# Kernel optimization log

Measured on AMD Instinct MI355X. Metric: run time of the kernel, lower is better.

Reference implementation:

```python
import jax, jax.numpy as jnp
import numpy as np

EMBED_DIM = 1024
NUM_HEADS = 16
HEAD_DIM = EMBED_DIM // NUM_HEADS
THETA = 10000.0


def setup_inputs() -> dict:
    key = jax.random.key(0)
    ks = jax.random.split(key, 5)
    B, S, E = 2, 2048, EMBED_DIM
    x = jax.random.normal(ks[0], (B, S, E), dtype=jnp.float32)
    s = 1.0 / np.sqrt(E)
    Wq = jax.random.normal(ks[1], (E, E), dtype=jnp.float32) * s
    Wk = jax.random.normal(ks[2], (E, E), dtype=jnp.float32) * s
    Wv = jax.random.normal(ks[3], (E, E), dtype=jnp.float32) * s
    Wo = jax.random.normal(ks[4], (E, E), dtype=jnp.float32) * s
    bo = jnp.zeros((E,), dtype=jnp.float32)
    return {"x": x, "Wq": Wq, "Wk": Wk, "Wv": Wv, "Wo": Wo, "bo": bo}


def _apply_rope(t, cos, sin):
    # t: (B, H, S, D); cos, sin: (S, D/2)
    t1 = t[..., 0::2]
    t2 = t[..., 1::2]
    r1 = t1 * cos - t2 * sin
    r2 = t1 * sin + t2 * cos
    # interleave back: (..., D/2, 2) -> (..., D)
    return jnp.stack([r1, r2], axis=-1).reshape(t.shape)


def reference(x, Wq, Wk, Wv, Wo, bo):
    B, S, E = x.shape
    H, D = NUM_HEADS, HEAD_DIM
    scale = D ** -0.5

    # projections (torch Linear: y = x @ W.T)
    q = (x @ Wq.T).reshape(B, S, H, D).transpose(0, 2, 1, 3)
    k = (x @ Wk.T).reshape(B, S, H, D).transpose(0, 2, 1, 3)
    v = (x @ Wv.T).reshape(B, S, H, D).transpose(0, 2, 1, 3)

    # fixed RoPE freqs (temporal, non-learned)
    freqs = 1.0 / THETA ** (jnp.arange(0, D, 2, dtype=jnp.float32) / D)  # (D/2,)
    pos = jnp.arange(S, dtype=jnp.float32)
    angles = pos[:, None] * freqs[None, :]  # (S, D/2)
    cos, sin = jnp.cos(angles), jnp.sin(angles)

    q = _apply_rope(q, cos, sin)
    k = _apply_rope(k, cos, sin)

    attn = jnp.einsum('bhqd,bhkd->bhqk', q, k) * scale
    attn = jax.nn.softmax(attn, axis=-1)
    out = jnp.einsum('bhqk,bhkd->bhqd', attn, v)
    out = out.transpose(0, 2, 1, 3).reshape(B, S, E)
    return out @ Wo.T + bo
```

## Files before the change

### kernel.cpp

```cpp
#include <hip/hip_runtime.h>


typedef __attribute__((ext_vector_type(8))) short bf16x8;
typedef __attribute__((ext_vector_type(4))) float f32x4;
typedef unsigned short u16;
typedef unsigned int u32;

#define MFMA(a, b, c) __builtin_amdgcn_mfma_f32_16x16x32_bf16((a), (b), (c), 0, 0, 0)

#define GLOAD16(g, l)                                                        \
  __builtin_amdgcn_global_load_lds((const __attribute__((address_space(1))) void*)(g), \
                                   (__attribute__((address_space(3))) void*)(l), 16, 0, 0)

__device__ __forceinline__ float bf2f(u16 u) {
  union { u32 i; float f; } v; v.i = ((u32)u) << 16; return v.f;
}
__device__ __forceinline__ u16 f2bf(float f) {
  union { float f; u32 i; } v; v.f = f;
  u32 x = v.i;
  return (u16)((x + 0x7fffu + ((x >> 16) & 1u)) >> 16);
}
__device__ __forceinline__ float exp2a(float x) {
  float y;
  asm("v_exp_f32 %0, %1" : "=v"(y) : "v"(x));
  return y;
}
__device__ __forceinline__ u32 cvtpk(float a, float b) {
  u32 w;
  asm("v_cvt_pk_bf16_f32 %0, %1, %2" : "=v"(w) : "v"(a), "v"(b));
  return w;
}

__global__ __launch_bounds__(256) void prep_kernel(
    const float* __restrict__ x, const float* __restrict__ Wq, const float* __restrict__ Wk,
    const float* __restrict__ Wv, const float* __restrict__ Wo, u16* __restrict__ xb,
    u16* __restrict__ Wqb, u16* __restrict__ Wkb, u16* __restrict__ Wvb, u16* __restrict__ Wob,
    float* __restrict__ cosT, float* __restrict__ sinT) {
  int bid = blockIdx.x;
  if (bid < 4096) {
    int i = bid * 256 + threadIdx.x;
    const float* src;
    u16* dst;
    int r, sel;
    if (i < 524288) {
      src = x; dst = xb; r = i; sel = -1;
    } else {
      int k = i - 524288;
      sel = k >> 17;
      r = k & 131071;
      src = sel == 0 ? Wq : sel == 1 ? Wk : sel == 2 ? Wv : Wo;
      dst = sel == 0 ? Wqb : sel == 1 ? Wkb : sel == 2 ? Wvb : Wob;
    }
    const float4* p = (const float4*)src + 2 * (size_t)r;
    float4 a = p[0], b = p[1];
    bf16x8 o;
    o[0] = (short)f2bf(a.x); o[1] = (short)f2bf(a.y);
    o[2] = (short)f2bf(a.z); o[3] = (short)f2bf(a.w);
    o[4] = (short)f2bf(b.x); o[5] = (short)f2bf(b.y);
    o[6] = (short)f2bf(b.z); o[7] = (short)f2bf(b.w);
    int outr = r;
    if (sel == 0 || sel == 1) {
      int row = r >> 7, kc = r & 127;
      int h = row >> 6, dd = row & 63;
      int u = dd & 1, pp = dd >> 1, half = pp >> 4, c = pp & 15;
      int g = 16 * (2 * half + u) + c;
      outr = (h * 64 + g) * 128 + kc;
    }
    *(bf16x8*)(dst + 8 * (size_t)outr) = o;
  } else {
    int i = (bid - 4096) * 256 + threadIdx.x;
    int p = i >> 11, s = i & 2047;
    float freq = powf(10000.0f, -(float)(2 * p) / 64.0f);
    float ang = (float)s * freq;
    cosT[i] = cosf(ang);
    sinT[i] = sinf(ang);
  }
}

template <int MODE>
__global__ __launch_bounds__(256) void gemm_bt_kernel(
    const u16* __restrict__ A, const u16* __restrict__ B0, const u16* __restrict__ B1,
    const u16* __restrict__ B2, u16* __restrict__ Qo, u16* __restrict__ Ko,
    u16* __restrict__ VT, const float* __restrict__ cosT, const float* __restrict__ sinT,
    float* __restrict__ Cf, const float* __restrict__ bias, int Ntot) {
  const int K = 1024;
  const int tid = threadIdx.x, lane = tid & 63, wid = tid >> 6;
  const int wr = wid >> 1, wc = wid & 1;
  const int wg = blockIdx.y * gridDim.x + blockIdx.x;
  const int xcd = wg & 7, loc = wg >> 3;
  const int mt = xcd * 4 + (loc & 3);
  const int nt = loc >> 2;
  const int m0 = mt * 128;
  const int n0 = nt * 128;
  const u16* Bt;
  int nloc0, sel;
  if (MODE == 0) {
    sel = nt >> 3;
    Bt = sel == 0 ? B0 : (sel == 1 ? B1 : B2);
    nloc0 = n0 & 1023;
  } else {
    sel = 0;
    Bt = B0;
    nloc0 = n0;
  }

  constexpr int NB = (MODE == 1) ? 2 : 1;
  __shared__ u16 As[NB][128 * 64];
  __shared__ u16 Bs[NB][128 * 64];

  f32x4 acc[4][4];
#pragma unroll
  for (int i = 0; i < 4; i++)
#pragma unroll
    for (int j = 0; j < 4; j++) acc[i][j] = f32x4{0.f, 0.f, 0.f, 0.f};

  const int strow = tid >> 3;
  const int sgcol0 = (tid & 7) * 8;

  auto stage = [&](int k0, int bf) {
#pragma unroll
    for (int p = 0; p < 4; ++p) {
      int row = p * 32 + strow;
      int gcol = sgcol0 ^ ((row & 7) << 3);
      const u16* ga = A + (size_t)(m0 + row) * K + k0 + gcol;
      const u16* gb = Bt + (size_t)(nloc0 + row) * K + k0 + gcol;
      u16* la = As[bf] + (p * 256 + wid * 64) * 8;
      u16* lb = Bs[bf] + (p * 256 + wid * 64) * 8;
      GLOAD16(ga, la);
      GLOAD16(gb, lb);
    }
  };

  auto compute = [&](int bf) {
#pragma unroll
    for (int kk = 0; kk < 2; ++kk) {
      bf16x8 af[4], bfr[4];
#pragma unroll
      for (int i = 0; i < 4; ++i) {
        int row = wr * 64 + i * 16 + (lane & 15);
        int col = (kk * 32 + (lane >> 4) * 8) ^ ((row & 7) << 3);
        af[i] = *(const bf16x8*)(As[bf] + row * 64 + col);
      }
#pragma unroll
      for (int j = 0; j < 4; ++j) {
        int row = wc * 64 + j * 16 + (lane & 15);
        int col = (kk * 32 + (lane >> 4) * 8) ^ ((row & 7) << 3);
        bfr[j] = *(const bf16x8*)(Bs[bf] + row * 64 + col);
      }
#pragma unroll
      for (int i = 0; i < 4; ++i)
#pragma unroll
        for (int j = 0; j < 4; ++j) acc[i][j] = MFMA(af[i], bfr[j], acc[i][j]);
    }
  };

  if (MODE == 1) {
    stage(0, 0);
    for (int kt = 0; kt < 16; ++kt) {
      __syncthreads();
      if (kt + 1 < 16) stage((kt + 1) * 64, (kt + 1) & 1);
      compute(kt & 1);
    }
  } else {
    for (int k0 = 0; k0 < K; k0 += 64) {
      stage(k0, 0);
      __syncthreads();
      compute(0);
      __syncthreads();
    }
  }

  if (MODE == 1) {
#pragma unroll
    for (int i = 0; i < 4; ++i)
#pragma unroll
      for (int j = 0; j < 4; ++j)
#pragma unroll
        for (int r = 0; r < 4; ++r) {
          int row = m0 + wr * 64 + i * 16 + (lane >> 4) * 4 + r;
          int col = n0 + wc * 64 + j * 16 + (lane & 15);
          Cf[(size_t)row * Ntot + col] = acc[i][j][r] + bias[col];
        }
    return;
  }

  const int c = lane & 15;
  const int hh = (nloc0 + wc * 64) >> 6;
  if (sel < 2) {
    u16* dst = sel == 0 ? Qo : Ko;
    const float mul = sel == 0 ? 0.18033688f : 1.0f;
#pragma unroll
    for (int i = 0; i < 4; ++i) {
      int rowb = m0 + wr * 64 + i * 16 + (lane >> 4) * 4;
      int s = rowb & 2047, b = rowb >> 11;
      size_t obase = ((size_t)(b * 16 + hh) * 2048 + s) * 64;
#pragma unroll
      for (int half = 0; half < 2; ++half) {
        int p = half * 16 + c;
        float4 c4 = *(const float4*)(cosT + p * 2048 + s);
        float4 s4 = *(const float4*)(sinT + p * 2048 + s);
#pragma unroll
        for (int r = 0; r < 4; ++r) {
          float t1 = acc[i][2 * half][r], t2 = acc[i][2 * half + 1][r];
          float cc = (&c4.x)[r], ss = (&s4.x)[r];
          float r0 = (t1 * cc - t2 * ss) * mul;
          float r1 = (t1 * ss + t2 * cc) * mul;
          u32 pk = (u32)f2bf(r0) | ((u32)f2bf(r1) << 16);
          *(u32*)(dst + obase + (size_t)r * 64 + 2 * p) = pk;
        }
      }
    }
  } else {
#pragma unroll
    for (int i = 0; i < 4; ++i) {
      int rowb = m0 + wr * 64 + i * 16 + (lane >> 4) * 4;
      int s = rowb & 2047, b = rowb >> 11;
#pragma unroll
      for (int j = 0; j < 4; ++j) {
        int dd = j * 16 + c;
        ushort4 pk;
        pk.x = f2bf(acc[i][j][0]);
        pk.y = f2bf(acc[i][j][1]);
        pk.z = f2bf(acc[i][j][2]);
        pk.w = f2bf(acc[i][j][3]);
        *(ushort4*)(VT + ((size_t)(b * 16 + hh) * 64 + dd) * 2048 + s) = pk;
      }
    }
  }
}

__global__ __launch_bounds__(256) void attn_kernel(
    const u16* __restrict__ Q, const u16* __restrict__ Kk, const u16* __restrict__ VT,
    u16* __restrict__ O) {
  const int wg = blockIdx.y * gridDim.x + blockIdx.x;
  const int xcd = wg & 7, loc = wg >> 3;
  const int qt = loc & 15;
  const int bh = xcd * 4 + (loc >> 4);
  const int tid = threadIdx.x, lane = tid & 63, wid = tid >> 6;
  const int b = bh >> 4, h = bh & 15;
  const int hi = lane >> 4, c = lane & 15;
  const float CEXP = 34.6246810f;

  __shared__ u16 Ks[2][64 * 64];
  __shared__ u16 Vs[2][64 * 64];
  __shared__ char Ps[4][16 * 288];

  const int qrow0 = qt * 128 + wid * 32;
  bf16x8 qf[2][2];
#pragma unroll
  for (int g = 0; g < 2; ++g) {
    const size_t qbase = ((size_t)bh * 2048 + qrow0 + g * 16 + c) * 64;
    qf[g][0] = *(const bf16x8*)(Q + qbase + hi * 8);
    qf[g][1] = *(const bf16x8*)(Q + qbase + 32 + hi * 8);
  }

  f32x4 o[2][4];
#pragma unroll
  for (int g = 0; g < 2; ++g)
#pragma unroll
    for (int j = 0; j < 4; ++j) o[g][j] = f32x4{0.f, 0.f, 0.f, 0.f};
  float lsum[2] = {0.f, 0.f};

  const u16* Kb = Kk + (size_t)bh * 2048 * 64;
  const u16* Vb = VT + (size_t)bh * 64 * 2048;

  const int strow = tid >> 3;
  const int sgc0 = (tid & 7) * 8;
  auto stage = [&](int t, int buf) {
#pragma unroll
    for (int p = 0; p < 2; ++p) {
      int row = p * 32 + strow;
      int gcol = sgc0 ^ ((row & 7) << 3);
      const u16* gk = Kb + (size_t)(t * 64 + row) * 64 + gcol;
      const u16* gv = Vb + (size_t)row * 2048 + t * 64 + gcol;
      u16* lk = Ks[buf] + (p * 256 + wid * 64) * 8;
      u16* lv = Vs[buf] + (p * 256 + wid * 64) * 8;
      GLOAD16(gk, lk);
      GLOAD16(gv, lv);
    }
  };

  stage(0, 0);
  char* Pw = &Ps[wid][0];
  const int pwb = hi * 288 + c * 8;
  const int prb = hi * 576 + c * 8;
  for (int t = 0; t < 32; ++t) {
    const int buf = t & 1;
    __syncthreads();
    if (t + 1 < 32) stage(t + 1, buf ^ 1);

    bf16x8 kf[2][4];
#pragma unroll
    for (int kk = 0; kk < 2; ++kk)
#pragma unroll
      for (int j = 0; j < 4; ++j) {
        int row = j * 16 + c;
        int col = (kk * 32 + hi * 8) ^ ((row & 7) << 3);
        kf[kk][j] = *(const bf16x8*)(Ks[buf] + row * 64 + col);
      }

    f32x4 sc[2][4];
#pragma unroll
    for (int g = 0; g < 2; ++g)
#pragma unroll
      for (int j = 0; j < 4; ++j) sc[g][j] = f32x4{0.f, 0.f, 0.f, 0.f};
    __builtin_amdgcn_s_setprio(1);
#pragma unroll
    for (int kk = 0; kk < 2; ++kk)
#pragma unroll
      for (int g = 0; g < 2; ++g)
#pragma unroll
        for (int j = 0; j < 4; ++j) sc[g][j] = MFMA(kf[kk][j], qf[g][kk], sc[g][j]);
    __builtin_amdgcn_s_setprio(0);

#pragma unroll
    for (int g = 0; g < 2; ++g)
#pragma unroll
      for (int j = 0; j < 4; ++j) {
        float e0 = exp2a(sc[g][j][0] - CEXP);
        float e1 = exp2a(sc[g][j][1] - CEXP);
        float e2 = exp2a(sc[g][j][2] - CEXP);
        float e3 = exp2a(sc[g][j][3] - CEXP);
        lsum[g] += (e0 + e1) + (e2 + e3);
        uint2 w;
        w.x = cvtpk(e0, e1);
        w.y = cvtpk(e2, e3);
        *(uint2*)(Pw + pwb + j * 1152 + g * 128) = w;
      }

    bf16x8 vf[2][4];
#pragma unroll
    for (int kk = 0; kk < 2; ++kk)
#pragma unroll
      for (int j = 0; j < 4; ++j) {
        int vrow = j * 16 + c;
        int vcol = (kk * 32 + hi * 8) ^ ((vrow & 7) << 3);
        vf[kk][j] = *(const bf16x8*)(Vs[buf] + vrow * 64 + vcol);
      }

    __builtin_amdgcn_s_setprio(1);
#pragma unroll
    for (int g = 0; g < 2; ++g)
#pragma unroll
      for (int kk = 0; kk < 2; ++kk) {
        uint2 a = *(const uint2*)(Pw + prb + kk * 2304 + g * 128);
        uint2 bb = *(const uint2*)(Pw + prb + kk * 2304 + g * 128 + 288);
        union { u32 w[4]; bf16x8 v; } pu;
        pu.w[0] = a.x; pu.w[1] = a.y; pu.w[2] = bb.x; pu.w[3] = bb.y;
#pragma unroll
        for (int jd = 0; jd < 4; ++jd) o[g][jd] = MFMA(pu.v, vf[kk][jd], o[g][jd]);
      }
    __builtin_amdgcn_s_setprio(0);
  }

  float linv[2][4];
#pragma unroll
  for (int g = 0; g < 2; ++g) {
    lsum[g] += __shfl_xor(lsum[g], 16, 64);
    lsum[g] += __shfl_xor(lsum[g], 32, 64);
#pragma unroll
    for (int r = 0; r < 4; ++r) {
      float L = __shfl(lsum[g], 4 * hi + r, 64);
      linv[g][r] = __frcp_rn(L);
    }
  }

#pragma unroll
  for (int g = 0; g < 2; ++g)
#pragma unroll
    for (int jd = 0; jd < 4; ++jd)
#pragma unroll
      for (int r = 0; r < 4; ++r) {
        int srow = qrow0 + g * 16 + hi * 4 + r;
        int col = h * 64 + jd * 16 + c;
        float val = o[g][jd][r] * linv[g][r];
        O[(size_t)(b * 2048 + srow) * 1024 + col] = f2bf(val);
      }
}

extern "C" void kernel_launch(void* const* d_in, const int* in_sizes, int n_in,
                              void* d_out, int out_size, void* d_ws, size_t ws_size,
                              hipStream_t stream) {
  const float* x = (const float*)d_in[0];
  const float* Wq = (const float*)d_in[1];
  const float* Wk = (const float*)d_in[2];
  const float* Wv = (const float*)d_in[3];
  const float* Wo = (const float*)d_in[4];
  const float* bo = (const float*)d_in[5];

  char* ws = (char*)d_ws;
  size_t off = 0;
  auto carve = [&](size_t bytes) {
    void* pp = ws + off;
    off += (bytes + 255) & ~(size_t)255;
    return pp;
  };
  u16* xb = (u16*)carve(4194304ull * 2);
  u16* Wqb = (u16*)carve(1048576ull * 2);
  u16* Wkb = (u16*)carve(1048576ull * 2);
  u16* Wvb = (u16*)carve(1048576ull * 2);
  u16* Wob = (u16*)carve(1048576ull * 2);
  float* cosT = (float*)carve(65536ull * 4);
  float* sinT = (float*)carve(65536ull * 4);
  u16* q_r = (u16*)carve(4194304ull * 2);
  u16* k_r = (u16*)carve(4194304ull * 2);
  u16* vT = (u16*)carve(4194304ull * 2);
  u16* attn_out = (u16*)carve(4194304ull * 2);

  prep_kernel<<<4352, 256, 0, stream>>>(x, Wq, Wk, Wv, Wo, xb, Wqb, Wkb, Wvb, Wob, cosT, sinT);
  gemm_bt_kernel<0><<<dim3(24, 32), 256, 0, stream>>>(xb, Wqb, Wkb, Wvb, q_r, k_r, vT, cosT,
                                                      sinT, nullptr, nullptr, 3072);
  attn_kernel<<<dim3(16, 32), 256, 0, stream>>>(q_r, k_r, vT, attn_out);
  gemm_bt_kernel<1><<<dim3(8, 32), 256, 0, stream>>>(attn_out, Wob, nullptr, nullptr, nullptr,
                                                     nullptr, nullptr, nullptr, nullptr,
                                                     (float*)d_out, bo, 1024);
}
```

Baseline: 200.0 us.

## Split out-projection into 64x128-tile kernel and compute softmax row sums via MFMA

Replaces the templated GEMM with a dedicated QKV kernel and a separate output-projection kernel that uses 64x128 tiles and a 512-block grid. The smaller tiles double the workgroup count so more CUs are busy for the 4096x1024 output GEMM. In attention, the exp offset is folded into the accumulator initialisation, and the row sums are computed by an extra MFMA against a ones vector instead of scalar adds plus cross-lane shuffles. This moves VALU and shuffle work onto the matrix unit at the cost of one extra MFMA per P block, and the row sums now come from bf16-rounded probabilities.

```diff
diff --git a/kernel.cpp b/kernel.cpp
--- a/kernel.cpp
+++ b/kernel.cpp
@@ -12,9 +12,6 @@
   __builtin_amdgcn_global_load_lds((const __attribute__((address_space(1))) void*)(g), \
                                    (__attribute__((address_space(3))) void*)(l), 16, 0, 0)
 
-__device__ __forceinline__ float bf2f(u16 u) {
-  union { u32 i; float f; } v; v.i = ((u32)u) << 16; return v.f;
-}
 __device__ __forceinline__ u16 f2bf(float f) {
   union { float f; u32 i; } v; v.f = f;
   u32 x = v.i;
@@ -77,12 +74,10 @@
   }
 }
 
-template <int MODE>
-__global__ __launch_bounds__(256) void gemm_bt_kernel(
+__global__ __launch_bounds__(256) void gemm_qkv_kernel(
     const u16* __restrict__ A, const u16* __restrict__ B0, const u16* __restrict__ B1,
     const u16* __restrict__ B2, u16* __restrict__ Qo, u16* __restrict__ Ko,
-    u16* __restrict__ VT, const float* __restrict__ cosT, const float* __restrict__ sinT,
-    float* __restrict__ Cf, const float* __restrict__ bias, int Ntot) {
+    u16* __restrict__ VT, const float* __restrict__ cosT, const float* __restrict__ sinT) {
   const int K = 1024;
   const int tid = threadIdx.x, lane = tid & 63, wid = tid >> 6;
   const int wr = wid >> 1, wc = wid & 1;
@@ -92,21 +87,12 @@
   const int nt = loc >> 2;
   const int m0 = mt * 128;
   const int n0 = nt * 128;
-  const u16* Bt;
-  int nloc0, sel;
-  if (MODE == 0) {
-    sel = nt >> 3;
-    Bt = sel == 0 ? B0 : (sel == 1 ? B1 : B2);
-    nloc0 = n0 & 1023;
-  } else {
-    sel = 0;
-    Bt = B0;
-    nloc0 = n0;
-  }
-
-  constexpr int NB = (MODE == 1) ? 2 : 1;
-  __shared__ u16 As[NB][128 * 64];
-  __shared__ u16 Bs[NB][128 * 64];
+  const int sel = nt >> 3;
+  const u16* Bt = sel == 0 ? B0 : (sel == 1 ? B1 : B2);
+  const int nloc0 = n0 & 1023;
+
+  __shared__ u16 As[128 * 64];
+  __shared__ u16 Bs[128 * 64];
 
   f32x4 acc[4][4];
 #pragma unroll
@@ -117,21 +103,23 @@
   const int strow = tid >> 3;
   const int sgcol0 = (tid & 7) * 8;
 
-  auto stage = [&](int k0, int bf) {
+  auto stage = [&](int k0) {
 #pragma unroll
     for (int p = 0; p < 4; ++p) {
       int row = p * 32 + strow;
       int gcol = sgcol0 ^ ((row & 7) << 3);
       const u16* ga = A + (size_t)(m0 + row) * K + k0 + gcol;
       const u16* gb = Bt + (size_t)(nloc0 + row) * K + k0 + gcol;
-      u16* la = As[bf] + (p * 256 + wid * 64) * 8;
-      u16* lb = Bs[bf] + (p * 256 + wid * 64) * 8;
+      u16* la = As + (p * 256 + wid * 64) * 8;
+      u16* lb = Bs + (p * 256 + wid * 64) * 8;
       GLOAD16(ga, la);
       GLOAD16(gb, lb);
     }
   };
 
-  auto compute = [&](int bf) {
+  for (int k0 = 0; k0 < K; k0 += 64) {
+    stage(k0);
+    __syncthreads();
 #pragma unroll
     for (int kk = 0; kk < 2; ++kk) {
       bf16x8 af[4], bfr[4];
@@ -139,49 +127,20 @@
       for (int i = 0; i < 4; ++i) {
         int row = wr * 64 + i * 16 + (lane & 15);
         int col = (kk * 32 + (lane >> 4) * 8) ^ ((row & 7) << 3);
-        af[i] = *(const bf16x8*)(As[bf] + row * 64 + col);
+        af[i] = *(const bf16x8*)(As + row * 64 + col);
       }
 #pragma unroll
       for (int j = 0; j < 4; ++j) {
         int row = wc * 64 + j * 16 + (lane & 15);
         int col = (kk * 32 + (lane >> 4) * 8) ^ ((row & 7) << 3);
-        bfr[j] = *(const bf16x8*)(Bs[bf] + row * 64 + col);
+        bfr[j] = *(const bf16x8*)(Bs + row * 64 + col);
       }
 #pragma unroll
       for (int i = 0; i < 4; ++i)
 #pragma unroll
         for (int j = 0; j < 4; ++j) acc[i][j] = MFMA(af[i], bfr[j], acc[i][j]);
     }
-  };
-
-  if (MODE == 1) {
-    stage(0, 0);
-    for (int kt = 0; kt < 16; ++kt) {
-      __syncthreads();
-      if (kt + 1 < 16) stage((kt + 1) * 64, (kt + 1) & 1);
-      compute(kt & 1);
-    }
-  } else {
-    for (int k0 = 0; k0 < K; k0 += 64) {
-      stage(k0, 0);
-      __syncthreads();
-      compute(0);
-      __syncthreads();
-    }
-  }
-
-  if (MODE == 1) {
-#pragma unroll
-    for (int i = 0; i < 4; ++i)
-#pragma unroll
-      for (int j = 0; j < 4; ++j)
-#pragma unroll
-        for (int r = 0; r < 4; ++r) {
-          int row = m0 + wr * 64 + i * 16 + (lane >> 4) * 4 + r;
-          int col = n0 + wc * 64 + j * 16 + (lane & 15);
-          Cf[(size_t)row * Ntot + col] = acc[i][j][r] + bias[col];
-        }
-    return;
+    __syncthreads();
   }
 
   const int c = lane & 15;
@@ -227,6 +186,87 @@
       }
     }
   }
+}
+
+__global__ __launch_bounds__(256) void gemm_out_kernel(
+    const u16* __restrict__ A, const u16* __restrict__ Bw, float* __restrict__ Cf,
+    const float* __restrict__ bias) {
+  const int K = 1024, Ntot = 1024;
+  const int tid = threadIdx.x, lane = tid & 63, wid = tid >> 6;
+  const int wr = wid >> 1, wc = wid & 1;
+  const int wg = blockIdx.x;
+  const int xcd = wg & 7, loc = wg >> 3;
+  const int mt = xcd * 8 + (loc & 7);
+  const int nt = loc >> 3;
+  const int m0 = mt * 64, n0 = nt * 128;
+
+  __shared__ u16 As[2][64 * 64];
+  __shared__ u16 Bs[2][128 * 64];
+
+  f32x4 acc[2][4];
+#pragma unroll
+  for (int i = 0; i < 2; i++)
+#pragma unroll
+    for (int j = 0; j < 4; j++) acc[i][j] = f32x4{0.f, 0.f, 0.f, 0.f};
+
+  const int strow = tid >> 3;
+  const int sgcol0 = (tid & 7) * 8;
+
+  auto stage = [&](int k0, int bf) {
+#pragma unroll
+    for (int p = 0; p < 2; ++p) {
+      int row = p * 32 + strow;
+      int gcol = sgcol0 ^ ((row & 7) << 3);
+      GLOAD16(A + (size_t)(m0 + row) * K + k0 + gcol, As[bf] + (p * 256 + wid * 64) * 8);
+    }
+#pragma unroll
+    for (int p = 0; p < 4; ++p) {
+      int row = p * 32 + strow;
+      int gcol = sgcol0 ^ ((row & 7) << 3);
+      GLOAD16(Bw + (size_t)(n0 + row) * K + k0 + gcol, Bs[bf] + (p * 256 + wid * 64) * 8);
+    }
+  };
+
+  auto compute = [&](int bf) {
+#pragma unroll
+    for (int kk = 0; kk < 2; ++kk) {
+      bf16x8 af[2], bfr[4];
+#pragma unroll
+      for (int i = 0; i < 2; ++i) {
+        int row = wr * 32 + i * 16 + (lane & 15);
+        int col = (kk * 32 + (lane >> 4) * 8) ^ ((row & 7) << 3);
+        af[i] = *(const bf16x8*)(As[bf] + row * 64 + col);
+      }
+#pragma unroll
+      for (int j = 0; j < 4; ++j) {
+        int row = wc * 64 + j * 16 + (lane & 15);
+        int col = (kk * 32 + (lane >> 4) * 8) ^ ((row & 7) << 3);
+        bfr[j] = *(const bf16x8*)(Bs[bf] + row * 64 + col);
+      }
+#pragma unroll
+      for (int i = 0; i < 2; ++i)
+#pragma unroll
+        for (int j = 0; j < 4; ++j) acc[i][j] = MFMA(af[i], bfr[j], acc[i][j]);
+    }
+  };
+
+  stage(0, 0);
+  for (int kt = 0; kt < 16; ++kt) {
+    __syncthreads();
+    if (kt + 1 < 16) stage((kt + 1) * 64, (kt + 1) & 1);
+    compute(kt & 1);
+  }
+
+#pragma unroll
+  for (int i = 0; i < 2; ++i)
+#pragma unroll
+    for (int j = 0; j < 4; ++j)
+#pragma unroll
+      for (int r = 0; r < 4; ++r) {
+        int row = m0 + wr * 32 + i * 16 + (lane >> 4) * 4 + r;
+        int col = n0 + wc * 64 + j * 16 + (lane & 15);
+        Cf[(size_t)row * Ntot + col] = acc[i][j][r] + bias[col];
+      }
 }
 
 __global__ __launch_bounds__(256) void attn_kernel(
@@ -254,12 +294,16 @@
     qf[g][1] = *(const bf16x8*)(Q + qbase + 32 + hi * 8);
   }
 
+  bf16x8 ONES;
+#pragma unroll
+  for (int e = 0; e < 8; ++e) ONES[e] = (short)0x3F80;
+
   f32x4 o[2][4];
 #pragma unroll
   for (int g = 0; g < 2; ++g)
 #pragma unroll
     for (int j = 0; j < 4; ++j) o[g][j] = f32x4{0.f, 0.f, 0.f, 0.f};
-  float lsum[2] = {0.f, 0.f};
+  f32x4 ol[2] = {f32x4{0.f, 0.f, 0.f, 0.f}, f32x4{0.f, 0.f, 0.f, 0.f}};
 
   const u16* Kb = Kk + (size_t)bh * 2048 * 64;
   const u16* Vb = VT + (size_t)bh * 64 * 2048;
@@ -303,7 +347,7 @@
 #pragma unroll
     for (int g = 0; g < 2; ++g)
 #pragma unroll
-      for (int j = 0; j < 4; ++j) sc[g][j] = f32x4{0.f, 0.f, 0.f, 0.f};
+      for (int j = 0; j < 4; ++j) sc[g][j] = f32x4{-CEXP, -CEXP, -CEXP, -CEXP};
     __builtin_amdgcn_s_setprio(1);
 #pragma unroll
     for (int kk = 0; kk < 2; ++kk)
@@ -317,11 +361,10 @@
     for (int g = 0; g < 2; ++g)
 #pragma unroll
       for (int j = 0; j < 4; ++j) {
-        float e0 = exp2a(sc[g][j][0] - CEXP);
-        float e1 = exp2a(sc[g][j][1] - CEXP);
-        float e2 = exp2a(sc[g][j][2] - CEXP);
-        float e3 = exp2a(sc[g][j][3] - CEXP);
-        lsum[g] += (e0 + e1) + (e2 + e3);
+        float e0 = exp2a(sc[g][j][0]);
+        float e1 = exp2a(sc[g][j][1]);
+        float e2 = exp2a(sc[g][j][2]);
+        float e3 = exp2a(sc[g][j][3]);
         uint2 w;
         w.x = cvtpk(e0, e1);
         w.y = cvtpk(e2, e3);
@@ -347,35 +390,28 @@
         uint2 bb = *(const uint2*)(Pw + prb + kk * 2304 + g * 128 + 288);
         union { u32 w[4]; bf16x8 v; } pu;
         pu.w[0] = a.x; pu.w[1] = a.y; pu.w[2] = bb.x; pu.w[3] = bb.y;
+        ol[g] = MFMA(pu.v, ONES, ol[g]);
 #pragma unroll
         for (int jd = 0; jd < 4; ++jd) o[g][jd] = MFMA(pu.v, vf[kk][jd], o[g][jd]);
       }
     __builtin_amdgcn_s_setprio(0);
   }
 
-  float linv[2][4];
 #pragma unroll
   for (int g = 0; g < 2; ++g) {
-    lsum[g] += __shfl_xor(lsum[g], 16, 64);
-    lsum[g] += __shfl_xor(lsum[g], 32, 64);
-#pragma unroll
-    for (int r = 0; r < 4; ++r) {
-      float L = __shfl(lsum[g], 4 * hi + r, 64);
-      linv[g][r] = __frcp_rn(L);
-    }
-  }
-
-#pragma unroll
-  for (int g = 0; g < 2; ++g)
+    float linv[4];
+#pragma unroll
+    for (int r = 0; r < 4; ++r) linv[r] = __frcp_rn(ol[g][r]);
 #pragma unroll
     for (int jd = 0; jd < 4; ++jd)
 #pragma unroll
       for (int r = 0; r < 4; ++r) {
         int srow = qrow0 + g * 16 + hi * 4 + r;
         int col = h * 64 + jd * 16 + c;
-        float val = o[g][jd][r] * linv[g][r];
+        float val = o[g][jd][r] * linv[r];
         O[(size_t)(b * 2048 + srow) * 1024 + col] = f2bf(val);
       }
+  }
 }
 
 extern "C" void kernel_launch(void* const* d_in, const int* in_sizes, int n_in,
@@ -408,10 +444,7 @@
   u16* attn_out = (u16*)carve(4194304ull * 2);
 
   prep_kernel<<<4352, 256, 0, stream>>>(x, Wq, Wk, Wv, Wo, xb, Wqb, Wkb, Wvb, Wob, cosT, sinT);
-  gemm_bt_kernel<0><<<dim3(24, 32), 256, 0, stream>>>(xb, Wqb, Wkb, Wvb, q_r, k_r, vT, cosT,
-                                                      sinT, nullptr, nullptr, 3072);
+  gemm_qkv_kernel<<<dim3(24, 32), 256, 0, stream>>>(xb, Wqb, Wkb, Wvb, q_r, k_r, vT, cosT, sinT);
   attn_kernel<<<dim3(16, 32), 256, 0, stream>>>(q_r, k_r, vT, attn_out);
-  gemm_bt_kernel<1><<<dim3(8, 32), 256, 0, stream>>>(attn_out, Wob, nullptr, nullptr, nullptr,
-                                                     nullptr, nullptr, nullptr, nullptr,
-                                                     (float*)d_out, bo, 1024);
-}
+  gemm_out_kernel<<<512, 256, 0, stream>>>(attn_out, Wob, (float*)d_out, bo);
+}
```

Result: faster. 194.4 us (-2.8%).
